# Kernel tuning notes

Measured on AMD Instinct MI355X. Metric: run time of the kernel, lower is better.

The kernel has to match this reference:

```python
import jax, jax.numpy as jnp
import numpy as np

H = 512  # hidden_size


def _highway_lstm(x, lengths, Wi, bi, Ws, bs):
    B, T, D = x.shape
    # Precompute all input projections in one big GEMM: [B, T, 6H]
    pi = jnp.einsum('btd,kd->btk', x, Wi) + bi
    mask = jnp.arange(T)[None, :] < lengths[:, None]  # [B, T]

    def step(carry, inp):
        h, c = carry
        pi_t, m = inp                      # pi_t: [B, 6H], m: [B]
        ps = h @ Ws.T + bs                 # [B, 5H]
        i = jax.nn.sigmoid(pi_t[:, 0*H:1*H] + ps[:, 0*H:1*H])
        f = jax.nn.sigmoid(pi_t[:, 1*H:2*H] + ps[:, 1*H:2*H])
        g = jnp.tanh(pi_t[:, 2*H:3*H] + ps[:, 2*H:3*H])
        o = jax.nn.sigmoid(pi_t[:, 3*H:4*H] + ps[:, 3*H:4*H])
        c_new = i * g + f * c
        out = o * jnp.tanh(c_new)
        # highway gate blends LSTM output with linear input projection
        r = jax.nn.sigmoid(pi_t[:, 4*H:5*H] + ps[:, 4*H:5*H])
        out = r * out + (1.0 - r) * pi_t[:, 5*H:6*H]
        m2 = m[:, None]
        h_new = jnp.where(m2, out, h)      # hold state past sequence end
        c_new = jnp.where(m2, c_new, c)
        y = jnp.where(m2, out, jnp.zeros_like(out))  # packed-seq padding = 0
        return (h_new, c_new), y

    h0 = jnp.zeros((B, H), x.dtype)
    c0 = jnp.zeros((B, H), x.dtype)
    (hT, cT), ys = jax.lax.scan(step, (h0, c0),
                                (jnp.swapaxes(pi, 0, 1), mask.T))
    return jnp.swapaxes(ys, 0, 1), hT, cT  # outputs [B,T,H], final (h, c)


def setup_inputs() -> dict:
    key = jax.random.key(0)
    ks = jax.random.split(key, 4)
    B, T, D = 32, 512, 512
    x = jax.random.normal(ks[0], (B, T, D), dtype=jnp.float32)
    lengths = jax.random.randint(ks[1], (B,), 1, T + 1, dtype=jnp.int32)
    Wi = jax.random.normal(ks[2], (6 * H, D), dtype=jnp.float32) * 0.05
    bi = jnp.zeros((6 * H,), dtype=jnp.float32)
    Ws = jax.random.normal(ks[3], (5 * H, H), dtype=jnp.float32) * 0.05
    bs = jnp.zeros((5 * H,), dtype=jnp.float32)
    return {"x": x, "lengths": lengths, "Wi": Wi, "bi": bi, "Ws": Ws, "bs": bs}


def reference(x, lengths, Wi, bi, Ws, bs):
    return _highway_lstm(x, lengths, Wi, bi, Ws, bs)
```

## Files before the change

### kernel.cpp

```cpp
#include <hip/hip_runtime.h>
#include <stdint.h>

typedef __attribute__((ext_vector_type(8))) short short8;
typedef __attribute__((ext_vector_type(4))) float f32x4;
typedef unsigned long long u64;

constexpr int cB = 32, cT = 512, cD = 512, cH = 512;
constexpr int cKI = 6 * cH;
constexpr int NWG = 32;
constexpr int THR = 320;
constexpr int LDW = 40;
constexpr int HP  = 520;
constexpr int RNG = 3;
constexpr int FPAD = 16;

__device__ __forceinline__ float bf2f(unsigned short u) {
  union { unsigned int i; float f; } x; x.i = ((unsigned int)u) << 16; return x.f;
}
__device__ __forceinline__ unsigned short f2bf(float f) {
  union { float f; unsigned int i; } x; x.f = f;
  return (unsigned short)((x.i + 0x7fffu + ((x.i >> 16) & 1u)) >> 16);
}
__device__ __forceinline__ float sigm(float v) { return 1.0f / (1.0f + __expf(-v)); }
__device__ __forceinline__ float tanh_f(float v) { return 2.0f / (1.0f + __expf(-2.0f * v)) - 1.0f; }

__global__ __launch_bounds__(256) void gemm_pi(
    const float* __restrict__ x,
    const float* __restrict__ Wi,
    const float* __restrict__ bi,
    unsigned short* __restrict__ pi)
{
  __shared__ __align__(16) unsigned short Ai[128 * LDW];
  __shared__ __align__(16) unsigned short Bi[128 * LDW];

  const int tid = threadIdx.x;
  const int lane = tid & 63;
  const int w = tid >> 6;
  const int wm = w & 1, wn = w >> 1;
  const int k0 = blockIdx.x * 128;
  const int n0 = blockIdx.y * 128;

  f32x4 acc[4][4];
  #pragma unroll
  for (int i = 0; i < 4; i++)
    #pragma unroll
    for (int j = 0; j < 4; j++) acc[i][j] = (f32x4){0.f, 0.f, 0.f, 0.f};

  for (int kk = 0; kk < cD; kk += 32) {
    __syncthreads();
    #pragma unroll
    for (int it = 0; it < 4; it++) {
      int idx = tid + it * 256;
      int r = idx >> 3, ch = idx & 7;
      int na = n0 + r;
      int bb = na & 31, tt = na >> 5;
      float4 va = *(const float4*)(x + ((size_t)bb * cT + tt) * cD + kk + ch * 4);
      ushort4 pa; pa.x = f2bf(va.x); pa.y = f2bf(va.y); pa.z = f2bf(va.z); pa.w = f2bf(va.w);
      *(ushort4*)(Ai + r * LDW + ch * 4) = pa;
      float4 vb = *(const float4*)(Wi + (size_t)(k0 + r) * cD + kk + ch * 4);
      ushort4 pb; pb.x = f2bf(vb.x); pb.y = f2bf(vb.y); pb.z = f2bf(vb.z); pb.w = f2bf(vb.w);
      *(ushort4*)(Bi + r * LDW + ch * 4) = pb;
    }
    __syncthreads();

    short8 af[4], bfr[4];
    const int q = lane >> 4;
    #pragma unroll
    for (int mi = 0; mi < 4; mi++) {
      int m = wm * 64 + mi * 16 + (lane & 15);
      af[mi] = *(const short8*)(Ai + m * LDW + q * 8);
    }
    #pragma unroll
    for (int ni = 0; ni < 4; ni++) {
      int n = wn * 64 + ni * 16 + (lane & 15);
      bfr[ni] = *(const short8*)(Bi + n * LDW + q * 8);
    }
    #pragma unroll
    for (int mi = 0; mi < 4; mi++)
      #pragma unroll
      for (int ni = 0; ni < 4; ni++)
        acc[mi][ni] = __builtin_amdgcn_mfma_f32_16x16x32_bf16(af[mi], bfr[ni], acc[mi][ni], 0, 0, 0);
  }

  #pragma unroll
  for (int ni = 0; ni < 4; ni++) {
    int kl = wn * 64 + ni * 16 + (lane & 15);
    float bv = bi[k0 + kl];
    #pragma unroll
    for (int mi = 0; mi < 4; mi++) {
      int nl = wm * 64 + mi * 16 + (lane >> 4) * 4;
      int nb = n0 + nl;
      int b0 = nb & 31, tt = nb >> 5;
      f32x4 a = acc[mi][ni];
      unsigned short v0 = f2bf(a.x + bv), v1 = f2bf(a.y + bv);
      unsigned short v2 = f2bf(a.z + bv), v3 = f2bf(a.w + bv);
      uint2 pv; pv.x = (unsigned)v0 | ((unsigned)v1 << 16);
      pv.y = (unsigned)v2 | ((unsigned)v3 << 16);
      *(uint2*)(pi + ((size_t)tt * cKI + k0 + kl) * cB + b0) = pv;
    }
  }
}

__global__ __launch_bounds__(THR, 1) void lstm_rec(
    const unsigned short* __restrict__ pi,
    const float* __restrict__ Ws,
    const float* __restrict__ bs,
    const int* __restrict__ lengths,
    unsigned short* __restrict__ hbuf,
    int* __restrict__ flags,
    float* __restrict__ out)
{
  __shared__ __align__(16) unsigned short h_lds[32 * HP];
  __shared__ __align__(16) unsigned short piL[RNG * 6 * 16 * 32];
  __shared__ __align__(16) float ps_lds[5 * 16 * 36];
  __shared__ __align__(16) float c_lds[16 * 32];
  __shared__ __align__(16) unsigned short hstg[16 * 32];
  __shared__ float bs_lds[80];
  __shared__ int len_lds[32];

  const int tid = threadIdx.x;
  const int lane = tid & 63;
  const int w = tid >> 6;
  const int wg = blockIdx.x;
  const int ci0 = wg * 16;
  const int mc = lane & 15;
  const int kq = lane >> 4;

  short8 bfrag[16];
  {
    const float* wsrow = Ws + (size_t)(w * cH + ci0 + mc) * cH;
    #pragma unroll
    for (int kt = 0; kt < 16; kt++) {
      float4 f0 = *(const float4*)(wsrow + kt * 32 + kq * 8);
      float4 f1 = *(const float4*)(wsrow + kt * 32 + kq * 8 + 4);
      short8 pk;
      pk[0] = (short)f2bf(f0.x); pk[1] = (short)f2bf(f0.y);
      pk[2] = (short)f2bf(f0.z); pk[3] = (short)f2bf(f0.w);
      pk[4] = (short)f2bf(f1.x); pk[5] = (short)f2bf(f1.y);
      pk[6] = (short)f2bf(f1.z); pk[7] = (short)f2bf(f1.w);
      bfrag[kt] = pk;
    }
  }
  if (tid < 80) bs_lds[tid] = bs[(tid >> 4) * cH + ci0 + (tid & 15)];
  if (tid < cB) len_lds[tid] = lengths[tid];
  for (int q = tid; q < 16 * 32; q += THR) c_lds[q] = 0.0f;
  for (int q = tid; q < 32 * HP / 4; q += THR) ((u64*)h_lds)[q] = 0ull;

  for (int s = 0; s < 2; s++) {
    const unsigned short* pit = pi + (size_t)s * cKI * cB;
    for (int j = tid; j < 384; j += THR) {
      int g = j >> 6, rem = j & 63, c = rem >> 2, q = rem & 3;
      uint4 v = *(const uint4*)(pit + ((size_t)g * cH + ci0 + c) * cB + q * 8);
      *(uint4*)(piL + s * 3072 + (g * 16 + c) * 32 + q * 8) = v;
    }
  }
  if (tid < 128) {
    int b = tid >> 2, q = tid & 3;
    u64* hd0 = (u64*)hbuf;
    __hip_atomic_store(hd0 + b * 128 + (ci0 >> 2) + q, 0ull, __ATOMIC_RELAXED, __HIP_MEMORY_SCOPE_AGENT);
  }
  __syncthreads();
  if (tid == 0)
    __hip_atomic_store(&flags[wg * FPAD], 1, __ATOMIC_RELAXED, __HIP_MEMORY_SCOPE_AGENT);
  if (tid < 32) {
    while (true) {
      int f = __hip_atomic_load(&flags[tid * FPAD], __ATOMIC_RELAXED, __HIP_MEMORY_SCOPE_AGENT);
      if (__all(f >= 1)) break;
    }
  }
  __syncthreads();

  for (int t = 0; t < cT; t++) {
    u64 hv[13];
    if (t > 0) {
      u64* hs = (u64*)(hbuf + (size_t)(t & 1) * cB * cH);
      #pragma unroll
      for (int k = 0; k < 13; k++) {
        int idx = tid + k * THR;
        if (idx < 4096)
          hv[k] = __hip_atomic_load(hs + idx, __ATOMIC_RELAXED, __HIP_MEMORY_SCOPE_AGENT);
      }
    }
    uint4 pv0, pv1;
    const bool pf = (t + 2) < cT;
    const int slot_w = (t + 2) % RNG;
    if (pf) {
      const unsigned short* pit = pi + (size_t)(t + 2) * cKI * cB;
      { int g = tid >> 6, rem = tid & 63, c = rem >> 2, q = rem & 3;
        pv0 = *(const uint4*)(pit + ((size_t)g * cH + ci0 + c) * cB + q * 8); }
      int j1 = tid + THR;
      if (j1 < 384) { int g = j1 >> 6, rem = j1 & 63, c = rem >> 2, q = rem & 3;
        pv1 = *(const uint4*)(pit + ((size_t)g * cH + ci0 + c) * cB + q * 8); }
    }
    if (t > 0) {
      #pragma unroll
      for (int k = 0; k < 13; k++) {
        int idx = tid + k * THR;
        if (idx < 4096) {
          int b = idx >> 7, ch = idx & 127;
          *(u64*)(h_lds + b * HP + ch * 4) = hv[k];
        }
      }
    }
    __syncthreads();

    f32x4 acc0 = (f32x4){0.f,0.f,0.f,0.f}, acc1 = (f32x4){0.f,0.f,0.f,0.f};
    #pragma unroll
    for (int kt = 0; kt < 16; kt++) {
      int kc = kt * 4 + kq;
      short8 a0 = *(const short8*)(h_lds + mc * HP + kc * 8);
      short8 a1 = *(const short8*)(h_lds + (16 + mc) * HP + kc * 8);
      acc0 = __builtin_amdgcn_mfma_f32_16x16x32_bf16(a0, bfrag[kt], acc0, 0, 0, 0);
      acc1 = __builtin_amdgcn_mfma_f32_16x16x32_bf16(a1, bfrag[kt], acc1, 0, 0, 0);
    }
    {
      int r0 = kq * 4;
      *(f32x4*)(ps_lds + (w * 16 + mc) * 36 + r0) = acc0;
      *(f32x4*)(ps_lds + (w * 16 + mc) * 36 + r0 + 16) = acc1;
    }
    if (pf) {
      { int g = tid >> 6, rem = tid & 63, c = rem >> 2, q = rem & 3;
        *(uint4*)(piL + slot_w * 3072 + (g * 16 + c) * 32 + q * 8) = pv0; }
      int j1 = tid + THR;
      if (j1 < 384) { int g = j1 >> 6, rem = j1 & 63, c = rem >> 2, q = rem & 3;
        *(uint4*)(piL + slot_w * 3072 + (g * 16 + c) * 32 + q * 8) = pv1; }
    }
    __syncthreads();

    const unsigned short* pl = piL + (t % RNG) * 3072;
    #pragma unroll
    for (int u = 0; u < 2; u++) {
      int idx = tid + u * THR;
      if (idx < 512) {
        int b = idx & 31, c = idx >> 5;
        int col = ci0 + c;
        float a_i = bf2f(pl[(0*16 + c)*32 + b]) + ps_lds[(0*16 + c)*36 + b] + bs_lds[0*16 + c];
        float a_f = bf2f(pl[(1*16 + c)*32 + b]) + ps_lds[(1*16 + c)*36 + b] + bs_lds[1*16 + c];
        float a_g = bf2f(pl[(2*16 + c)*32 + b]) + ps_lds[(2*16 + c)*36 + b] + bs_lds[2*16 + c];
        float a_o = bf2f(pl[(3*16 + c)*32 + b]) + ps_lds[(3*16 + c)*36 + b] + bs_lds[3*16 + c];
        float a_r = bf2f(pl[(4*16 + c)*32 + b]) + ps_lds[(4*16 + c)*36 + b] + bs_lds[4*16 + c];
        float p5  = bf2f(pl[(5*16 + c)*32 + b]);
        float gi = sigm(a_i), gf = sigm(a_f), gg = tanh_f(a_g), go = sigm(a_o), gr = sigm(a_r);
        float cold = c_lds[c * 32 + b];
        float cn = gi * gg + gf * cold;
        float ov = go * tanh_f(cn);
        ov = gr * ov + (1.0f - gr) * p5;
        bool m = (t < len_lds[b]);
        float hold = bf2f(h_lds[b * HP + col]);
        float hn = m ? ov : hold;
        c_lds[c * 32 + b] = m ? cn : cold;
        hstg[c * 32 + b] = f2bf(hn);
        out[((size_t)b * cT + t) * cH + col] = m ? ov : 0.0f;
        if (t == cT - 1)
          out[(size_t)cB * cT * cH + (size_t)b * cH + col] = hn;
      }
    }
    if (t + 1 < cT) {
      __syncthreads();
      if (tid < 128) {
        int b = tid >> 2, q = tid & 3;
        u64 pk = (u64)hstg[(q*4 + 0)*32 + b] | ((u64)hstg[(q*4 + 1)*32 + b] << 16)
               | ((u64)hstg[(q*4 + 2)*32 + b] << 32) | ((u64)hstg[(q*4 + 3)*32 + b] << 48);
        u64* hd = (u64*)(hbuf + (size_t)((t + 1) & 1) * cB * cH);
        __hip_atomic_store(hd + b * 128 + (ci0 >> 2) + q, pk, __ATOMIC_RELAXED, __HIP_MEMORY_SCOPE_AGENT);
      }
      __syncthreads();
      if (tid == 0)
        __hip_atomic_store(&flags[wg * FPAD], t + 2, __ATOMIC_RELAXED, __HIP_MEMORY_SCOPE_AGENT);
      if (tid < 32) {
        while (true) {
          int f = __hip_atomic_load(&flags[tid * FPAD], __ATOMIC_RELAXED, __HIP_MEMORY_SCOPE_AGENT);
          if (__all(f >= t + 2)) break;
        }
      }
      __syncthreads();
    }
  }

  #pragma unroll
  for (int u = 0; u < 2; u++) {
    int idx = tid + u * THR;
    if (idx < 512) {
      int b = idx & 31, c = idx >> 5;
      out[(size_t)cB * cT * cH + (size_t)cB * cH + (size_t)b * cH + ci0 + c] = c_lds[c * 32 + b];
    }
  }
}

extern "C" void kernel_launch(void* const* d_in, const int* in_sizes, int n_in,
                              void* d_out, int out_size, void* d_ws, size_t ws_size,
                              hipStream_t stream) {
  const float* x       = (const float*)d_in[0];
  const int* lengths   = (const int*)d_in[1];
  const float* Wi      = (const float*)d_in[2];
  const float* bi      = (const float*)d_in[3];
  const float* Ws      = (const float*)d_in[4];
  const float* bs      = (const float*)d_in[5];
  float* out = (float*)d_out;

  char* ws = (char*)d_ws;
  int* flags = (int*)ws;
  unsigned short* hbuf = (unsigned short*)(ws + 4096);
  unsigned short* pi   = (unsigned short*)(ws + (1 << 20));

  hipMemsetAsync(flags, 0, NWG * FPAD * sizeof(int), stream);
  dim3 grid1(cKI / 128, (cB * cT) / 128);
  gemm_pi<<<grid1, 256, 0, stream>>>(x, Wi, bi, pi);
  lstm_rec<<<NWG, THR, 0, stream>>>(pi, Ws, bs, lengths, hbuf, flags, out);
}
```

Before: 2.007 ms.

## Co-locate recurrent workgroups on one XCD and use L2-scoped sync

Launches 256 blocks and has each read its XCD id from a hardware register, then elects the first XCD to collect 32 blocks; those 32 become the recurrent workers and the rest exit. With all workers sharing one L2, per-step h exchange and flag polling use workgroup-scope stores and sc0 loads that bypass only L1, which is meant to avoid the slower device-coherent path across XCDs. A startup handshake checks that the cheap coherence actually works and otherwise falls back to the original agent-scope atomics. It relies on undocumented behaviour (hardware register layout, cache bits) and adds startup election overhead plus extra launched blocks.

```diff
diff --git a/kernel.cpp b/kernel.cpp
--- a/kernel.cpp
+++ b/kernel.cpp
@@ -3,16 +3,20 @@
 
 typedef __attribute__((ext_vector_type(8))) short short8;
 typedef __attribute__((ext_vector_type(4))) float f32x4;
+typedef __attribute__((ext_vector_type(4))) unsigned int u32x4;
 typedef unsigned long long u64;
 
 constexpr int cB = 32, cT = 512, cD = 512, cH = 512;
 constexpr int cKI = 6 * cH;
 constexpr int NWG = 32;
+constexpr int NLAUNCH = 256;
 constexpr int THR = 320;
 constexpr int LDW = 40;
 constexpr int HP  = 520;
 constexpr int RNG = 3;
 constexpr int FPAD = 16;
+constexpr int MAGIC = 0x5AFE;
+
 
 __device__ __forceinline__ float bf2f(unsigned short u) {
   union { unsigned int i; float f; } x; x.i = ((unsigned int)u) << 16; return x.f;
@@ -23,6 +27,20 @@
 }
 __device__ __forceinline__ float sigm(float v) { return 1.0f / (1.0f + __expf(-v)); }
 __device__ __forceinline__ float tanh_f(float v) { return 2.0f / (1.0f + __expf(-2.0f * v)) - 1.0f; }
+
+__device__ __forceinline__ void st_wg_i32(int* p, int v) {
+  __hip_atomic_store(p, v, __ATOMIC_RELAXED, __HIP_MEMORY_SCOPE_WORKGROUP);
+}
+__device__ __forceinline__ void st_wg_u64(u64* p, u64 v) {
+  __hip_atomic_store(p, v, __ATOMIC_RELAXED, __HIP_MEMORY_SCOPE_WORKGROUP);
+}
+__device__ __forceinline__ int ld_flag_sc0(const int* p) {
+  int v;
+  asm volatile("global_load_dword %0, %1, off sc0\n\t"
+               "s_waitcnt vmcnt(0)"
+               : "=&v"(v) : "v"(p) : "memory");
+  return v;
+}
 
 __global__ __launch_bounds__(256) void gemm_pi(
     const float* __restrict__ x,
@@ -117,11 +135,41 @@
   __shared__ __align__(16) unsigned short hstg[16 * 32];
   __shared__ float bs_lds[80];
   __shared__ int len_lds[32];
+  __shared__ int s_slot;
+  __shared__ int s_fast;
 
   const int tid = threadIdx.x;
+
+  {
+    int* ecnt = flags + 512;
+    int* ewin = flags + 528;
+    if (tid == 0) {
+      int xcd = (int)__builtin_amdgcn_s_getreg(20 | (31 << 11)) & 15;
+      int slot = __hip_atomic_fetch_add(&ecnt[xcd], 1, __ATOMIC_RELAXED, __HIP_MEMORY_SCOPE_AGENT);
+      if (slot == NWG - 1) {
+        int e = 0;
+        __hip_atomic_compare_exchange_strong(ewin, &e, xcd + 1,
+            __ATOMIC_RELAXED, __ATOMIC_RELAXED, __HIP_MEMORY_SCOPE_AGENT);
+      }
+      int win, it = 0;
+      while ((win = __hip_atomic_load(ewin, __ATOMIC_RELAXED, __HIP_MEMORY_SCOPE_AGENT)) == 0) {
+        if (++it > 20000) {
+          int e = 0;
+          __hip_atomic_compare_exchange_strong(ewin, &e, 999,
+              __ATOMIC_RELAXED, __ATOMIC_RELAXED, __HIP_MEMORY_SCOPE_AGENT);
+        }
+        __builtin_amdgcn_s_sleep(8);
+      }
+      if (win == 999) s_slot = ((int)blockIdx.x < NWG) ? (int)blockIdx.x : -1;
+      else            s_slot = (((win - 1) == xcd) && (slot < NWG)) ? slot : -1;
+    }
+    __syncthreads();
+  }
+  const int wg = s_slot;
+  if (wg < 0) return;
+
   const int lane = tid & 63;
   const int w = tid >> 6;
-  const int wg = blockIdx.x;
   const int ci0 = wg * 16;
   const int mc = lane & 15;
   const int kq = lane >> 4;
@@ -156,9 +204,23 @@
   }
   if (tid < 128) {
     int b = tid >> 2, q = tid & 3;
-    u64* hd0 = (u64*)hbuf;
-    __hip_atomic_store(hd0 + b * 128 + (ci0 >> 2) + q, 0ull, __ATOMIC_RELAXED, __HIP_MEMORY_SCOPE_AGENT);
-  }
+    st_wg_u64((u64*)hbuf + b * 128 + (ci0 >> 2) + q, 0ull);
+  }
+
+  if (tid == 0) st_wg_i32(flags + 544 + wg * FPAD, MAGIC);
+  __syncthreads();
+  int okflag = 1;
+  if (tid < 32) {
+    const int* pp = flags + 544 + tid * FPAD;
+    int it = 0;
+    while (true) {
+      int v = ld_flag_sc0(pp);
+      if (__all(v == MAGIC)) break;
+      if (++it > 2000) { okflag = 0; break; }
+    }
+  }
+  if (tid == 0)
+    __hip_atomic_fetch_add(flags + 529, okflag, __ATOMIC_RELAXED, __HIP_MEMORY_SCOPE_AGENT);
   __syncthreads();
   if (tid == 0)
     __hip_atomic_store(&flags[wg * FPAD], 1, __ATOMIC_RELAXED, __HIP_MEMORY_SCOPE_AGENT);
@@ -168,17 +230,42 @@
       if (__all(f >= 1)) break;
     }
   }
+  if (tid == 0)
+    s_fast = (__hip_atomic_load(flags + 529, __ATOMIC_RELAXED, __HIP_MEMORY_SCOPE_AGENT) == NWG) ? 1 : 0;
   __syncthreads();
+  const bool fast = (s_fast != 0);
 
   for (int t = 0; t < cT; t++) {
+    u32x4 ha[8];
     u64 hv[13];
     if (t > 0) {
-      u64* hs = (u64*)(hbuf + (size_t)(t & 1) * cB * cH);
-      #pragma unroll
-      for (int k = 0; k < 13; k++) {
-        int idx = tid + k * THR;
-        if (idx < 4096)
-          hv[k] = __hip_atomic_load(hs + idx, __ATOMIC_RELAXED, __HIP_MEMORY_SCOPE_AGENT);
+      if (fast) {
+        if (tid < 256) {
+          const u32x4* hs = (const u32x4*)(hbuf + (size_t)(t & 1) * cB * cH) + tid;
+          asm volatile(
+            "global_load_dwordx4 %0, %8, off sc0\n\t"
+            "global_load_dwordx4 %1, %9, off sc0\n\t"
+            "global_load_dwordx4 %2, %10, off sc0\n\t"
+            "global_load_dwordx4 %3, %11, off sc0\n\t"
+            "global_load_dwordx4 %4, %12, off sc0\n\t"
+            "global_load_dwordx4 %5, %13, off sc0\n\t"
+            "global_load_dwordx4 %6, %14, off sc0\n\t"
+            "global_load_dwordx4 %7, %15, off sc0\n\t"
+            "s_waitcnt vmcnt(0)"
+            : "=&v"(ha[0]), "=&v"(ha[1]), "=&v"(ha[2]), "=&v"(ha[3]),
+              "=&v"(ha[4]), "=&v"(ha[5]), "=&v"(ha[6]), "=&v"(ha[7])
+            : "v"(hs), "v"(hs + 256), "v"(hs + 512), "v"(hs + 768),
+              "v"(hs + 1024), "v"(hs + 1280), "v"(hs + 1536), "v"(hs + 1792)
+            : "memory");
+        }
+      } else {
+        u64* hs = (u64*)(hbuf + (size_t)(t & 1) * cB * cH);
+        #pragma unroll
+        for (int k = 0; k < 13; k++) {
+          int idx = tid + k * THR;
+          if (idx < 4096)
+            hv[k] = __hip_atomic_load(hs + idx, __ATOMIC_RELAXED, __HIP_MEMORY_SCOPE_AGENT);
+        }
       }
     }
     uint4 pv0, pv1;
@@ -193,12 +280,23 @@
         pv1 = *(const uint4*)(pit + ((size_t)g * cH + ci0 + c) * cB + q * 8); }
     }
     if (t > 0) {
-      #pragma unroll
-      for (int k = 0; k < 13; k++) {
-        int idx = tid + k * THR;
-        if (idx < 4096) {
-          int b = idx >> 7, ch = idx & 127;
-          *(u64*)(h_lds + b * HP + ch * 4) = hv[k];
+      if (fast) {
+        if (tid < 256) {
+          #pragma unroll
+          for (int k = 0; k < 8; k++) {
+            int idx = tid + k * 256;
+            int b = idx >> 6, ch = idx & 63;
+            *(u32x4*)(h_lds + b * HP + ch * 8) = ha[k];
+          }
+        }
+      } else {
+        #pragma unroll
+        for (int k = 0; k < 13; k++) {
+          int idx = tid + k * THR;
+          if (idx < 4096) {
+            int b = idx >> 7, ch = idx & 127;
+            *(u64*)(h_lds + b * HP + ch * 4) = hv[k];
+          }
         }
       }
     }
@@ -261,16 +359,27 @@
         int b = tid >> 2, q = tid & 3;
         u64 pk = (u64)hstg[(q*4 + 0)*32 + b] | ((u64)hstg[(q*4 + 1)*32 + b] << 16)
                | ((u64)hstg[(q*4 + 2)*32 + b] << 32) | ((u64)hstg[(q*4 + 3)*32 + b] << 48);
-        u64* hd = (u64*)(hbuf + (size_t)((t + 1) & 1) * cB * cH);
-        __hip_atomic_store(hd + b * 128 + (ci0 >> 2) + q, pk, __ATOMIC_RELAXED, __HIP_MEMORY_SCOPE_AGENT);
+        u64* hd = (u64*)(hbuf + (size_t)((t + 1) & 1) * cB * cH) + b * 128 + (ci0 >> 2) + q;
+        if (fast) st_wg_u64(hd, pk);
+        else __hip_atomic_store(hd, pk, __ATOMIC_RELAXED, __HIP_MEMORY_SCOPE_AGENT);
       }
       __syncthreads();
-      if (tid == 0)
-        __hip_atomic_store(&flags[wg * FPAD], t + 2, __ATOMIC_RELAXED, __HIP_MEMORY_SCOPE_AGENT);
+      if (tid == 0) {
+        if (fast) st_wg_i32(flags + wg * FPAD, t + 2);
+        else __hip_atomic_store(&flags[wg * FPAD], t + 2, __ATOMIC_RELAXED, __HIP_MEMORY_SCOPE_AGENT);
+      }
       if (tid < 32) {
-        while (true) {
-          int f = __hip_atomic_load(&flags[tid * FPAD], __ATOMIC_RELAXED, __HIP_MEMORY_SCOPE_AGENT);
-          if (__all(f >= t + 2)) break;
+        if (fast) {
+          const int* fp = flags + tid * FPAD;
+          while (true) {
+            int f = ld_flag_sc0(fp);
+            if (__all(f >= t + 2)) break;
+          }
+        } else {
+          while (true) {
+            int f = __hip_atomic_load(&flags[tid * FPAD], __ATOMIC_RELAXED, __HIP_MEMORY_SCOPE_AGENT);
+            if (__all(f >= t + 2)) break;
+          }
         }
       }
       __syncthreads();
@@ -300,11 +409,11 @@
 
   char* ws = (char*)d_ws;
   int* flags = (int*)ws;
-  unsigned short* hbuf = (unsigned short*)(ws + 4096);
+  unsigned short* hbuf = (unsigned short*)(ws + 8192);
   unsigned short* pi   = (unsigned short*)(ws + (1 << 20));
 
-  hipMemsetAsync(flags, 0, NWG * FPAD * sizeof(int), stream);
+  hipMemsetAsync(flags, 0, 8192, stream);
   dim3 grid1(cKI / 128, (cB * cT) / 128);
   gemm_pi<<<grid1, 256, 0, stream>>>(x, Wi, bi, pi);
-  lstm_rec<<<NWG, THR, 0, stream>>>(pi, Ws, bs, lengths, hbuf, flags, out);
-}
+  lstm_rec<<<NLAUNCH, THR, 0, stream>>>(pi, Ws, bs, lengths, hbuf, flags, out);
+}
```

New measurement: 3.151 ms. 1.57x slower.

## Fuse input-projection GEMM into recurrent kernel with per-timestep readiness flags

Applied to the files above, without the earlier changes.

Merges the input-projection GEMM and the recurrent LSTM kernel into one launch. The first 32 blocks run the recurrence while the remaining blocks compute GEMM tiles and bump per-tile counters. The recurrent blocks poll those counters before prefetching upcoming timesteps, so the recurrence can start before the whole GEMM finishes. The change also writes h directly to global memory through shuffle-packed 32-bit atomics, dropping the staging buffer and one barrier, and moves the output stores after the flag publish. It adds spin-loop timeouts, and correctness relies on the GEMM blocks being scheduled alongside the recurrent ones, which puts deadlock-free forward progress at risk.

```diff
diff --git a/kernel.cpp b/kernel.cpp
--- a/kernel.cpp
+++ b/kernel.cpp
@@ -9,10 +9,19 @@
 constexpr int cKI = 6 * cH;
 constexpr int NWG = 32;
 constexpr int THR = 320;
-constexpr int LDW = 40;
 constexpr int HP  = 520;
 constexpr int RNG = 3;
+constexpr int PIP = 40;
 constexpr int FPAD = 16;
+constexpr int GK = 24, GN = 128;
+
+constexpr int OFF_PIL  = 32 * HP * 2;
+constexpr int OFF_PS   = OFF_PIL + RNG * 6 * 16 * PIP * 2;
+constexpr int OFF_C    = OFF_PS + 5 * 16 * 36 * 4;
+constexpr int OFF_BS   = OFF_C + 512 * 4;
+constexpr int OFF_LEN  = OFF_BS + 80 * 4;
+constexpr int OFF_MISC = OFF_LEN + 32 * 4;
+constexpr int SMEM_SZ  = OFF_MISC + 16;
 
 __device__ __forceinline__ float bf2f(unsigned short u) {
   union { unsigned int i; float f; } x; x.i = ((unsigned int)u) << 16; return x.f;
@@ -24,103 +33,102 @@
 __device__ __forceinline__ float sigm(float v) { return 1.0f / (1.0f + __expf(-v)); }
 __device__ __forceinline__ float tanh_f(float v) { return 2.0f / (1.0f + __expf(-2.0f * v)) - 1.0f; }
 
-__global__ __launch_bounds__(256) void gemm_pi(
+__global__ __launch_bounds__(THR, 1) void fused_lstm(
     const float* __restrict__ x,
     const float* __restrict__ Wi,
     const float* __restrict__ bi,
-    unsigned short* __restrict__ pi)
-{
-  __shared__ __align__(16) unsigned short Ai[128 * LDW];
-  __shared__ __align__(16) unsigned short Bi[128 * LDW];
-
-  const int tid = threadIdx.x;
-  const int lane = tid & 63;
-  const int w = tid >> 6;
-  const int wm = w & 1, wn = w >> 1;
-  const int k0 = blockIdx.x * 128;
-  const int n0 = blockIdx.y * 128;
-
-  f32x4 acc[4][4];
-  #pragma unroll
-  for (int i = 0; i < 4; i++)
-    #pragma unroll
-    for (int j = 0; j < 4; j++) acc[i][j] = (f32x4){0.f, 0.f, 0.f, 0.f};
-
-  for (int kk = 0; kk < cD; kk += 32) {
-    __syncthreads();
-    #pragma unroll
-    for (int it = 0; it < 4; it++) {
-      int idx = tid + it * 256;
-      int r = idx >> 3, ch = idx & 7;
-      int na = n0 + r;
-      int bb = na & 31, tt = na >> 5;
-      float4 va = *(const float4*)(x + ((size_t)bb * cT + tt) * cD + kk + ch * 4);
-      ushort4 pa; pa.x = f2bf(va.x); pa.y = f2bf(va.y); pa.z = f2bf(va.z); pa.w = f2bf(va.w);
-      *(ushort4*)(Ai + r * LDW + ch * 4) = pa;
-      float4 vb = *(const float4*)(Wi + (size_t)(k0 + r) * cD + kk + ch * 4);
-      ushort4 pb; pb.x = f2bf(vb.x); pb.y = f2bf(vb.y); pb.z = f2bf(vb.z); pb.w = f2bf(vb.w);
-      *(ushort4*)(Bi + r * LDW + ch * 4) = pb;
-    }
-    __syncthreads();
-
-    short8 af[4], bfr[4];
-    const int q = lane >> 4;
-    #pragma unroll
-    for (int mi = 0; mi < 4; mi++) {
-      int m = wm * 64 + mi * 16 + (lane & 15);
-      af[mi] = *(const short8*)(Ai + m * LDW + q * 8);
-    }
-    #pragma unroll
-    for (int ni = 0; ni < 4; ni++) {
-      int n = wn * 64 + ni * 16 + (lane & 15);
-      bfr[ni] = *(const short8*)(Bi + n * LDW + q * 8);
-    }
-    #pragma unroll
-    for (int mi = 0; mi < 4; mi++)
-      #pragma unroll
-      for (int ni = 0; ni < 4; ni++)
-        acc[mi][ni] = __builtin_amdgcn_mfma_f32_16x16x32_bf16(af[mi], bfr[ni], acc[mi][ni], 0, 0, 0);
-  }
-
-  #pragma unroll
-  for (int ni = 0; ni < 4; ni++) {
-    int kl = wn * 64 + ni * 16 + (lane & 15);
-    float bv = bi[k0 + kl];
-    #pragma unroll
-    for (int mi = 0; mi < 4; mi++) {
-      int nl = wm * 64 + mi * 16 + (lane >> 4) * 4;
-      int nb = n0 + nl;
-      int b0 = nb & 31, tt = nb >> 5;
-      f32x4 a = acc[mi][ni];
-      unsigned short v0 = f2bf(a.x + bv), v1 = f2bf(a.y + bv);
-      unsigned short v2 = f2bf(a.z + bv), v3 = f2bf(a.w + bv);
-      uint2 pv; pv.x = (unsigned)v0 | ((unsigned)v1 << 16);
-      pv.y = (unsigned)v2 | ((unsigned)v3 << 16);
-      *(uint2*)(pi + ((size_t)tt * cKI + k0 + kl) * cB + b0) = pv;
-    }
-  }
-}
-
-__global__ __launch_bounds__(THR, 1) void lstm_rec(
-    const unsigned short* __restrict__ pi,
     const float* __restrict__ Ws,
     const float* __restrict__ bs,
     const int* __restrict__ lengths,
+    unsigned short* __restrict__ pi,
     unsigned short* __restrict__ hbuf,
     int* __restrict__ flags,
     float* __restrict__ out)
 {
-  __shared__ __align__(16) unsigned short h_lds[32 * HP];
-  __shared__ __align__(16) unsigned short piL[RNG * 6 * 16 * 32];
-  __shared__ __align__(16) float ps_lds[5 * 16 * 36];
-  __shared__ __align__(16) float c_lds[16 * 32];
-  __shared__ __align__(16) unsigned short hstg[16 * 32];
-  __shared__ float bs_lds[80];
-  __shared__ int len_lds[32];
-
+  __shared__ __align__(16) unsigned char smem[SMEM_SZ];
   const int tid = threadIdx.x;
   const int lane = tid & 63;
   const int w = tid >> 6;
+
+  if (blockIdx.x >= NWG) {
+    const int gb = (int)blockIdx.x - NWG;
+    const int kb = gb % GK, nbk = gb / GK;
+    const int k0 = kb * 128, n0 = nbk * 128;
+    unsigned short* Ai = (unsigned short*)smem;
+    unsigned short* Bi = (unsigned short*)(smem + 10240);
+    const int wm = w & 1, wn = w >> 1;
+
+    f32x4 acc[4][4];
+    #pragma unroll
+    for (int i = 0; i < 4; i++)
+      #pragma unroll
+      for (int j = 0; j < 4; j++) acc[i][j] = (f32x4){0.f, 0.f, 0.f, 0.f};
+
+    for (int kk = 0; kk < cD; kk += 32) {
+      __syncthreads();
+      for (int idx = tid; idx < 1024; idx += THR) {
+        int r = idx >> 3, ch = idx & 7;
+        int na = n0 + r, bb = na & 31, tt = na >> 5;
+        float4 va = *(const float4*)(x + ((size_t)bb * cT + tt) * cD + kk + ch * 4);
+        ushort4 pa; pa.x = f2bf(va.x); pa.y = f2bf(va.y); pa.z = f2bf(va.z); pa.w = f2bf(va.w);
+        *(ushort4*)(Ai + r * PIP + ch * 4) = pa;
+        float4 vb = *(const float4*)(Wi + (size_t)(k0 + r) * cD + kk + ch * 4);
+        ushort4 pb; pb.x = f2bf(vb.x); pb.y = f2bf(vb.y); pb.z = f2bf(vb.z); pb.w = f2bf(vb.w);
+        *(ushort4*)(Bi + r * PIP + ch * 4) = pb;
+      }
+      __syncthreads();
+      if (w < 4) {
+        short8 af[4], bfr[4];
+        const int q = lane >> 4;
+        #pragma unroll
+        for (int mi = 0; mi < 4; mi++)
+          af[mi] = *(const short8*)(Ai + (wm * 64 + mi * 16 + (lane & 15)) * PIP + q * 8);
+        #pragma unroll
+        for (int ni = 0; ni < 4; ni++)
+          bfr[ni] = *(const short8*)(Bi + (wn * 64 + ni * 16 + (lane & 15)) * PIP + q * 8);
+        #pragma unroll
+        for (int mi = 0; mi < 4; mi++)
+          #pragma unroll
+          for (int ni = 0; ni < 4; ni++)
+            acc[mi][ni] = __builtin_amdgcn_mfma_f32_16x16x32_bf16(af[mi], bfr[ni], acc[mi][ni], 0, 0, 0);
+      }
+    }
+    if (w < 4) {
+      #pragma unroll
+      for (int ni = 0; ni < 4; ni++) {
+        int kl = wn * 64 + ni * 16 + (lane & 15);
+        float bv = bi[k0 + kl];
+        #pragma unroll
+        for (int mi = 0; mi < 4; mi++) {
+          int nl = wm * 64 + mi * 16 + (lane >> 4) * 4;
+          int nb = n0 + nl;
+          int b0 = nb & 31, tt = nb >> 5;
+          f32x4 a = acc[mi][ni];
+          unsigned short v0 = f2bf(a.x + bv), v1 = f2bf(a.y + bv);
+          unsigned short v2 = f2bf(a.z + bv), v3 = f2bf(a.w + bv);
+          u64 pk = (u64)v0 | ((u64)v1 << 16) | ((u64)v2 << 32) | ((u64)v3 << 48);
+          __hip_atomic_store((u64*)(pi + ((size_t)tt * cKI + k0 + kl) * cB + b0), pk,
+                             __ATOMIC_RELAXED, __HIP_MEMORY_SCOPE_AGENT);
+        }
+      }
+    }
+    __syncthreads();
+    if (tid == 0) {
+      __hip_atomic_fetch_add(flags + 512 + nbk, 1, __ATOMIC_RELAXED, __HIP_MEMORY_SCOPE_AGENT);
+      __hip_atomic_fetch_add(flags + 640, 1, __ATOMIC_RELAXED, __HIP_MEMORY_SCOPE_AGENT);
+    }
+    return;
+  }
+
+  unsigned short* h_lds  = (unsigned short*)smem;
+  unsigned short* piL    = (unsigned short*)(smem + OFF_PIL);
+  float* ps_lds          = (float*)(smem + OFF_PS);
+  float* c_lds           = (float*)(smem + OFF_C);
+  float* bs_lds          = (float*)(smem + OFF_BS);
+  int*   len_lds         = (int*)(smem + OFF_LEN);
+  int*   s_tr_p          = (int*)(smem + OFF_MISC);
+  int*   s_all_p         = s_tr_p + 1;
+
   const int wg = blockIdx.x;
   const int ci0 = wg * 16;
   const int mc = lane & 15;
@@ -143,34 +151,48 @@
   }
   if (tid < 80) bs_lds[tid] = bs[(tid >> 4) * cH + ci0 + (tid & 15)];
   if (tid < cB) len_lds[tid] = lengths[tid];
-  for (int q = tid; q < 16 * 32; q += THR) c_lds[q] = 0.0f;
+  for (int q = tid; q < 512; q += THR) c_lds[q] = 0.0f;
   for (int q = tid; q < 32 * HP / 4; q += THR) ((u64*)h_lds)[q] = 0ull;
+
+  if (tid == 0) {
+    *s_all_p = 0;
+    int it = 0;
+    while (__hip_atomic_load(flags + 512, __ATOMIC_RELAXED, __HIP_MEMORY_SCOPE_AGENT) < GK) {
+      __builtin_amdgcn_s_sleep(8);
+      if (++it > 1000000) { *s_all_p = 1; break; }
+    }
+    *s_tr_p = 4;
+  }
+  __syncthreads();
 
   for (int s = 0; s < 2; s++) {
     const unsigned short* pit = pi + (size_t)s * cKI * cB;
     for (int j = tid; j < 384; j += THR) {
       int g = j >> 6, rem = j & 63, c = rem >> 2, q = rem & 3;
       uint4 v = *(const uint4*)(pit + ((size_t)g * cH + ci0 + c) * cB + q * 8);
-      *(uint4*)(piL + s * 3072 + (g * 16 + c) * 32 + q * 8) = v;
+      *(uint4*)(piL + s * (6 * 16 * PIP) + (g * 16 + c) * PIP + q * 8) = v;
     }
   }
   if (tid < 128) {
     int b = tid >> 2, q = tid & 3;
-    u64* hd0 = (u64*)hbuf;
-    __hip_atomic_store(hd0 + b * 128 + (ci0 >> 2) + q, 0ull, __ATOMIC_RELAXED, __HIP_MEMORY_SCOPE_AGENT);
+    __hip_atomic_store((u64*)hbuf + b * 128 + (ci0 >> 2) + q, 0ull,
+                       __ATOMIC_RELAXED, __HIP_MEMORY_SCOPE_AGENT);
   }
   __syncthreads();
   if (tid == 0)
     __hip_atomic_store(&flags[wg * FPAD], 1, __ATOMIC_RELAXED, __HIP_MEMORY_SCOPE_AGENT);
   if (tid < 32) {
+    int itc = 0;
     while (true) {
       int f = __hip_atomic_load(&flags[tid * FPAD], __ATOMIC_RELAXED, __HIP_MEMORY_SCOPE_AGENT);
       if (__all(f >= 1)) break;
+      if (++itc > 20000000) break;
     }
   }
   __syncthreads();
 
   for (int t = 0; t < cT; t++) {
+    const bool last = (t == cT - 1);
     u64 hv[13];
     if (t > 0) {
       u64* hs = (u64*)(hbuf + (size_t)(t & 1) * cB * cH);
@@ -220,57 +242,85 @@
     }
     if (pf) {
       { int g = tid >> 6, rem = tid & 63, c = rem >> 2, q = rem & 3;
-        *(uint4*)(piL + slot_w * 3072 + (g * 16 + c) * 32 + q * 8) = pv0; }
+        *(uint4*)(piL + slot_w * (6 * 16 * PIP) + (g * 16 + c) * PIP + q * 8) = pv0; }
       int j1 = tid + THR;
       if (j1 < 384) { int g = j1 >> 6, rem = j1 & 63, c = rem >> 2, q = rem & 3;
-        *(uint4*)(piL + slot_w * 3072 + (g * 16 + c) * 32 + q * 8) = pv1; }
+        *(uint4*)(piL + slot_w * (6 * 16 * PIP) + (g * 16 + c) * PIP + q * 8) = pv1; }
     }
     __syncthreads();
 
-    const unsigned short* pl = piL + (t % RNG) * 3072;
+    const unsigned short* pl = piL + (t % RNG) * (6 * 16 * PIP);
+    unsigned* hb32 = (unsigned*)(hbuf + (size_t)((t + 1) & 1) * cB * cH);
+    float outv0 = 0.f, outv1 = 0.f;
     #pragma unroll
     for (int u = 0; u < 2; u++) {
       int idx = tid + u * THR;
       if (idx < 512) {
-        int b = idx & 31, c = idx >> 5;
+        int b = idx >> 4, c = idx & 15;
         int col = ci0 + c;
-        float a_i = bf2f(pl[(0*16 + c)*32 + b]) + ps_lds[(0*16 + c)*36 + b] + bs_lds[0*16 + c];
-        float a_f = bf2f(pl[(1*16 + c)*32 + b]) + ps_lds[(1*16 + c)*36 + b] + bs_lds[1*16 + c];
-        float a_g = bf2f(pl[(2*16 + c)*32 + b]) + ps_lds[(2*16 + c)*36 + b] + bs_lds[2*16 + c];
-        float a_o = bf2f(pl[(3*16 + c)*32 + b]) + ps_lds[(3*16 + c)*36 + b] + bs_lds[3*16 + c];
-        float a_r = bf2f(pl[(4*16 + c)*32 + b]) + ps_lds[(4*16 + c)*36 + b] + bs_lds[4*16 + c];
-        float p5  = bf2f(pl[(5*16 + c)*32 + b]);
+        float a_i = bf2f(pl[(0*16 + c)*PIP + b]) + ps_lds[(0*16 + c)*36 + b] + bs_lds[0*16 + c];
+        float a_f = bf2f(pl[(1*16 + c)*PIP + b]) + ps_lds[(1*16 + c)*36 + b] + bs_lds[1*16 + c];
+        float a_g = bf2f(pl[(2*16 + c)*PIP + b]) + ps_lds[(2*16 + c)*36 + b] + bs_lds[2*16 + c];
+        float a_o = bf2f(pl[(3*16 + c)*PIP + b]) + ps_lds[(3*16 + c)*36 + b] + bs_lds[3*16 + c];
+        float a_r = bf2f(pl[(4*16 + c)*PIP + b]) + ps_lds[(4*16 + c)*36 + b] + bs_lds[4*16 + c];
+        float p5  = bf2f(pl[(5*16 + c)*PIP + b]);
         float gi = sigm(a_i), gf = sigm(a_f), gg = tanh_f(a_g), go = sigm(a_o), gr = sigm(a_r);
-        float cold = c_lds[c * 32 + b];
+        float cold = c_lds[b * 16 + c];
         float cn = gi * gg + gf * cold;
         float ov = go * tanh_f(cn);
         ov = gr * ov + (1.0f - gr) * p5;
         bool m = (t < len_lds[b]);
         float hold = bf2f(h_lds[b * HP + col]);
         float hn = m ? ov : hold;
-        c_lds[c * 32 + b] = m ? cn : cold;
-        hstg[c * 32 + b] = f2bf(hn);
-        out[((size_t)b * cT + t) * cH + col] = m ? ov : 0.0f;
-        if (t == cT - 1)
+        c_lds[b * 16 + c] = m ? cn : cold;
+        float ovm = m ? ov : 0.0f;
+        unsigned short hus = f2bf(hn);
+        int pr = __shfl_down((int)(unsigned)hus, 1);
+        if (!last && (c & 1) == 0) {
+          unsigned up = (unsigned)hus | ((unsigned)pr << 16);
+          __hip_atomic_store(hb32 + ((b * cH + col) >> 1), up,
+                             __ATOMIC_RELAXED, __HIP_MEMORY_SCOPE_AGENT);
+        }
+        if (last) {
+          out[((size_t)b * cT + t) * cH + col] = ovm;
           out[(size_t)cB * cT * cH + (size_t)b * cH + col] = hn;
-      }
-    }
-    if (t + 1 < cT) {
-      __syncthreads();
-      if (tid < 128) {
-        int b = tid >> 2, q = tid & 3;
-        u64 pk = (u64)hstg[(q*4 + 0)*32 + b] | ((u64)hstg[(q*4 + 1)*32 + b] << 16)
-               | ((u64)hstg[(q*4 + 2)*32 + b] << 32) | ((u64)hstg[(q*4 + 3)*32 + b] << 48);
-        u64* hd = (u64*)(hbuf + (size_t)((t + 1) & 1) * cB * cH);
-        __hip_atomic_store(hd + b * 128 + (ci0 >> 2) + q, pk, __ATOMIC_RELAXED, __HIP_MEMORY_SCOPE_AGENT);
-      }
+        } else {
+          if (u == 0) outv0 = ovm; else outv1 = ovm;
+        }
+      }
+    }
+    if (!last) {
       __syncthreads();
       if (tid == 0)
         __hip_atomic_store(&flags[wg * FPAD], t + 2, __ATOMIC_RELAXED, __HIP_MEMORY_SCOPE_AGENT);
+      { int idx = tid;
+        if (idx < 512) { int b = idx >> 4, c = idx & 15;
+          out[((size_t)b * cT + t) * cH + ci0 + c] = outv0; }
+        idx = tid + THR;
+        if (idx < 512) { int b = idx >> 4, c = idx & 15;
+          out[((size_t)b * cT + t) * cH + ci0 + c] = outv1; } }
       if (tid < 32) {
+        int itc = 0;
         while (true) {
           int f = __hip_atomic_load(&flags[tid * FPAD], __ATOMIC_RELAXED, __HIP_MEMORY_SCOPE_AGENT);
           if (__all(f >= t + 2)) break;
+          if (++itc > 20000000) break;
+        }
+      }
+      if (tid == 64) {
+        if (!*s_all_p) {
+          int tr = *s_tr_p;
+          int need = t + 4; if (need > cT) need = cT;
+          int guard = 0;
+          while (tr < need) {
+            int tot = __hip_atomic_load(flags + 640, __ATOMIC_RELAXED, __HIP_MEMORY_SCOPE_AGENT);
+            if (tot >= GK * GN) { *s_all_p = 1; break; }
+            int v = __hip_atomic_load(flags + 512 + (tr >> 2), __ATOMIC_RELAXED, __HIP_MEMORY_SCOPE_AGENT);
+            if (v >= GK) { tr += 4; continue; }
+            __builtin_amdgcn_s_sleep(8);
+            if (++guard > 300000) { *s_all_p = 1; break; }
+          }
+          *s_tr_p = tr;
         }
       }
       __syncthreads();
@@ -281,8 +331,8 @@
   for (int u = 0; u < 2; u++) {
     int idx = tid + u * THR;
     if (idx < 512) {
-      int b = idx & 31, c = idx >> 5;
-      out[(size_t)cB * cT * cH + (size_t)cB * cH + (size_t)b * cH + ci0 + c] = c_lds[c * 32 + b];
+      int b = idx >> 4, c = idx & 15;
+      out[(size_t)cB * cT * cH + (size_t)cB * cH + (size_t)b * cH + ci0 + c] = c_lds[b * 16 + c];
     }
   }
 }
@@ -300,11 +350,10 @@
 
   char* ws = (char*)d_ws;
   int* flags = (int*)ws;
-  unsigned short* hbuf = (unsigned short*)(ws + 4096);
+  unsigned short* hbuf = (unsigned short*)(ws + 8192);
   unsigned short* pi   = (unsigned short*)(ws + (1 << 20));
 
-  hipMemsetAsync(flags, 0, NWG * FPAD * sizeof(int), stream);
-  dim3 grid1(cKI / 128, (cB * cT) / 128);
-  gemm_pi<<<grid1, 256, 0, stream>>>(x, Wi, bi, pi);
-  lstm_rec<<<NWG, THR, 0, stream>>>(pi, Ws, bs, lengths, hbuf, flags, out);
+  hipMemsetAsync(flags, 0, 8192, stream);
+  fused_lstm<<<NWG + GK * GN, THR, 0, stream>>>(x, Wi, bi, Ws, bs, lengths,
+                                                pi, hbuf, flags, out);
 }
```

Result: faster. 1.888 ms (-6.0%).
